# Kernel optimization log

Measured on AMD Instinct MI355X. Metric: run time of the kernel, lower is better.

Reference implementation:

```python
import jax, jax.numpy as jnp
import numpy as np

FEATURE_W = 1.0
TRIPLET_W = 1.0
MARGIN = 0.5
CE_W = 1.0
CE_TEMP = 0.1
DIR_W = 1.0
EPS_VALID = 1e-6
EPS_NORM = 1e-8


def setup_inputs() -> dict:
    key = jax.random.key(0)
    k1, k2, k3, k4, k5 = jax.random.split(key, 5)
    B, C, T, K = 8, 512, 1500, 4096
    return {
        "student_out": jax.random.normal(k1, (B, C, T), dtype=jnp.float32),
        "teacher_out": jax.random.normal(k2, (B, C, T), dtype=jnp.float32),
        "codebook": jax.random.normal(k3, (K, C), dtype=jnp.float32),
        "teacher_codes": jax.random.randint(k4, (B, T), 0, K, dtype=jnp.int64),
        "original_encoder_out": jax.random.normal(k5, (B, C, T), dtype=jnp.float32),
    }


def reference(student_out, teacher_out, codebook, teacher_codes, original_encoder_out):
    B, C, T = student_out.shape
    K = codebook.shape[0]
    N = B * T

    # ---- feature MSE ----
    feature_loss = jnp.mean((student_out - teacher_out) ** 2)

    # ---- triplet with hard negative mining ----
    z = jnp.transpose(student_out, (0, 2, 1)).reshape(N, C)  # (N, C)
    tgt = teacher_codes.reshape(N)
    # squared L2 distances (argmin-equivalent to cdist since sqrt is monotone)
    z2 = jnp.sum(z * z, axis=1, keepdims=True)            # (N, 1)
    c2 = jnp.sum(codebook * codebook, axis=1)             # (K,)
    d2 = z2 - 2.0 * (z @ codebook.T) + c2[None, :]        # (N, K)
    d2 = d2.at[jnp.arange(N), tgt].set(jnp.inf)           # exclude correct code
    hard_idx = jnp.argmin(d2, axis=1)                     # (N,)
    hard_negatives = codebook[hard_idx].reshape(B, T, C)

    anchor = jnp.transpose(teacher_out, (0, 2, 1))        # (B, T, C)
    positive = jnp.transpose(student_out, (0, 2, 1))
    d_pos = jnp.linalg.norm(anchor - positive, axis=-1)   # (B, T)
    d_neg = jnp.linalg.norm(anchor - hard_negatives, axis=-1)
    triplet_loss = jnp.mean(jax.nn.relu(d_pos - d_neg + MARGIN))

    # ---- CE over codebook (negative squared distance logits) ----
    logits = (2.0 * (z @ codebook.T) - c2[None, :]) / CE_TEMP  # (N, K)
    logp = jax.nn.log_softmax(logits, axis=-1)
    ce_loss = -jnp.mean(jnp.take_along_axis(logp, tgt[:, None], axis=1))

    # ---- direction-aware loss ----
    movement = jnp.transpose(student_out - original_encoder_out, (0, 2, 1)).reshape(N, C)
    direction = jnp.transpose(teacher_out - original_encoder_out, (0, 2, 1)).reshape(N, C)
    m_norm = jnp.linalg.norm(movement, axis=-1, keepdims=True)
    d_norm = jnp.linalg.norm(direction, axis=-1, keepdims=True)
    valid = (m_norm[:, 0] > EPS_VALID) & (d_norm[:, 0] > EPS_VALID)  # (N,)
    cos = jnp.sum((movement / (m_norm + EPS_NORM)) * (direction / (d_norm + EPS_NORM)), axis=-1)
    n_valid = jnp.sum(valid)
    dir_cos_loss = jnp.sum(jnp.where(valid, 1.0 - cos, 0.0)) / jnp.maximum(n_valid, 1).astype(cos.dtype)
    dir_mse = jnp.mean((student_out - teacher_out) ** 2)
    direction_loss = dir_mse + 1.0 * dir_cos_loss  # DirectionAwareLoss(direction_weight=1.0)

    total = (FEATURE_W * feature_loss + TRIPLET_W * triplet_loss
             + CE_W * ce_loss + DIR_W * direction_loss)
    return total
```

## Files before the change

kernel.cpp:

```cpp
#include <hip/hip_runtime.h>
#include <math.h>

#define NN 12000
#define NP 12032
#define CCD 512
#define KK 4096
#define TT 1500
#define S20F 28.853900817779268f
#define SC2F 14.426950408889634f
#define LN2F 0.6931471805599453f

typedef float f32x4 __attribute__((ext_vector_type(4)));
typedef __bf16 bf16x8 __attribute__((ext_vector_type(8)));

__device__ __forceinline__ ushort f2bf(float f){
  uint u = __float_as_uint(f);
  uint r = (u + 0x7fffu + ((u >> 16) & 1u)) >> 16;
  return (ushort)r;
}

typedef __attribute__((address_space(1))) const unsigned int g_u32;
typedef __attribute__((address_space(3))) unsigned int l_u32;
__device__ __forceinline__ void gload_lds16(const void* g, void* l){
  __builtin_amdgcn_global_load_lds((g_u32*)g, (l_u32*)l, 16, 0, 0);
}

__global__ __launch_bounds__(256) void k_prep_z(const float* __restrict__ src, ushort* __restrict__ dst){
  __shared__ float tile[64][65];
  int b = blockIdx.z, c0 = blockIdx.y*64, t0 = blockIdx.x*64;
  const float* sb = src + ((size_t)b*CCD + c0)*TT + t0;
  for (int i = 0; i < 16; ++i){
    int e = i*256 + threadIdx.x;
    int cl = e >> 6, tl = e & 63;
    if (t0 + tl < TT) tile[cl][tl] = sb[(size_t)cl*TT + tl];
  }
  __syncthreads();
  for (int i = 0; i < 16; ++i){
    int e = i*256 + threadIdx.x;
    int tl = e >> 6, cl = e & 63;
    if (t0 + tl < TT) dst[((size_t)b*TT + t0 + tl)*CCD + c0 + cl] = f2bf(tile[cl][tl]);
  }
}

__global__ __launch_bounds__(256) void k_prep_cb(const float* __restrict__ cb, ushort* __restrict__ cbsw){
  int id = blockIdx.x*256 + threadIdx.x;
  int l     = id & 63;
  int kstep = (id >> 6) & 15;
  int tile  = id >> 10;
  int code  = tile*16 + (l & 15);
  int cc    = kstep*32 + (l >> 4)*8;
  const float* src = cb + ((size_t)code*CCD + cc);
  float4 v0 = *(const float4*)src;
  float4 v1 = *(const float4*)(src + 4);
  uint4 o;
  o.x = (uint)f2bf(v0.x) | ((uint)f2bf(v0.y) << 16);
  o.y = (uint)f2bf(v0.z) | ((uint)f2bf(v0.w) << 16);
  o.z = (uint)f2bf(v1.x) | ((uint)f2bf(v1.y) << 16);
  o.w = (uint)f2bf(v1.z) | ((uint)f2bf(v1.w) << 16);
  ((uint4*)cbsw)[id] = o;
}

__global__ __launch_bounds__(256) void k_c2(const float* __restrict__ cb, float* __restrict__ c2s){
  int k = blockIdx.x*4 + (threadIdx.x >> 6);
  int lane = threadIdx.x & 63;
  const float4* p = (const float4*)(cb + (size_t)k*CCD);
  float s = 0.f;
  for (int i = lane; i < CCD/4; i += 64){
    float4 v = p[i];
    s += v.x*v.x + v.y*v.y + v.z*v.z + v.w*v.w;
  }
  for (int off=1; off<64; off<<=1) s += __shfl_xor(s, off);
  if (lane == 0) c2s[k] = s * SC2F;
}

__global__ __launch_bounds__(256) void k_dist(const ushort* __restrict__ zbf,
    const ushort* __restrict__ cbsw, const float* __restrict__ c2s,
    const int* __restrict__ codes, float4* __restrict__ pstate){
  __shared__ char cs[2*16384];
  int tid = threadIdx.x, w = tid >> 6, l = tid & 63;
  int lm = l & 15, k16 = l >> 4;
  int yk = blockIdx.x, xb = blockIdx.y;
  int n0 = xb * 128, kb = yk * 512;

  bf16x8 A0[16], A1[16];
  {
    const ushort* a0 = zbf + (size_t)(n0 + w*32 + lm)*CCD + k16*8;
#pragma unroll
    for (int u = 0; u < 16; ++u){
      A0[u] = *(const bf16x8*)(a0 + u*32);
      A1[u] = *(const bf16x8*)(a0 + 16*CCD + u*32);
    }
  }
  int tgt[8];
#pragma unroll
  for (int fi=0; fi<2; ++fi)
#pragma unroll
    for (int r=0; r<4; ++r){
      int n = n0 + w*32 + fi*16 + k16*4 + r;
      tgt[fi*4+r] = (n < NN) ? codes[n] : -1;
    }

  float m2[8], ss[8], bv[8]; int bi[8];
#pragma unroll
  for (int i=0;i<8;++i){ m2[i]=-3.0e38f; ss[i]=0.f; bv[i]=-3.0e38f; bi[i]=0x7fffffff; }

#define STAGE(tile, buf) { \
    const char* tb_ = (const char*)cbsw + ((size_t)(yk*32 + (tile)))*16384; \
    _Pragma("unroll") \
    for (int j_ = 0; j_ < 4; ++j_) \
      gload_lds16(tb_ + j_*4096 + tid*16, (buf) + j_*4096 + tid*16); }

  STAGE(0, cs)
  __syncthreads();

#pragma unroll 2
  for (int t = 0; t < 32; ++t){
    const char* cur = cs + (t & 1)*16384;
    char* nxt = cs + ((t + 1) & 1)*16384;
    if (t < 31) STAGE(t + 1, nxt)

    f32x4 a0e = (f32x4){0.f,0.f,0.f,0.f}, a0o = a0e, a1e = a0e, a1o = a0e;
    const char* pb = cur + l*16;
    __builtin_amdgcn_s_setprio(1);
#pragma unroll
    for (int ks = 0; ks < 16; ks += 2){
      bf16x8 b0 = *(const bf16x8*)(pb + ks*1024);
      bf16x8 b1 = *(const bf16x8*)(pb + ks*1024 + 1024);
      a0e = __builtin_amdgcn_mfma_f32_16x16x32_bf16(A0[ks],   b0, a0e, 0,0,0);
      a1e = __builtin_amdgcn_mfma_f32_16x16x32_bf16(A1[ks],   b0, a1e, 0,0,0);
      a0o = __builtin_amdgcn_mfma_f32_16x16x32_bf16(A0[ks+1], b1, a0o, 0,0,0);
      a1o = __builtin_amdgcn_mfma_f32_16x16x32_bf16(A1[ks+1], b1, a1o, 0,0,0);
    }
    __builtin_amdgcn_s_setprio(0);

    int c0g = kb + t*16 + lm;
    float c2r0 = c2s[c0g];
    f32x4 accf[2];
    accf[0] = a0e + a0o;
    accf[1] = a1e + a1o;
#pragma unroll
    for (int fi=0; fi<2; ++fi)
#pragma unroll
    for (int r=0; r<4; ++r){
      int i8 = fi*4 + r;
      float v0 = fmaf(accf[fi][r], S20F, -c2r0);
      if (c0g != tgt[i8] && v0 > bv[i8]){ bv[i8] = v0; bi[i8] = c0g; }
      float mn = fmaxf(m2[i8], v0);
      ss[i8] = ss[i8]*exp2f(m2[i8]-mn) + exp2f(v0-mn);
      m2[i8] = mn;
    }
    __syncthreads();
  }
#undef STAGE

#pragma unroll
  for (int off = 1; off < 16; off <<= 1){
#pragma unroll
    for (int i=0; i<8; ++i){
      float mo = __shfl_xor(m2[i], off);
      float so = __shfl_xor(ss[i], off);
      float bvo = __shfl_xor(bv[i], off);
      int  bio = __shfl_xor(bi[i], off);
      if (bvo > bv[i] || (bvo == bv[i] && bio < bi[i])){ bv[i] = bvo; bi[i] = bio; }
      float mn = fmaxf(m2[i], mo);
      ss[i] = ss[i]*exp2f(m2[i]-mn) + so*exp2f(mo-mn);
      m2[i] = mn;
    }
  }
  if (lm == 0){
#pragma unroll
    for (int fi=0; fi<2; ++fi)
#pragma unroll
    for (int r=0; r<4; ++r){
      int i8 = fi*4 + r;
      int row = w*32 + fi*16 + k16*4 + r;
      pstate[(size_t)yk*NP + n0 + row] =
          make_float4(m2[i8], ss[i8], bv[i8], __int_as_float(bi[i8]));
    }
  }
}

__global__ __launch_bounds__(256) void k_final(const float* __restrict__ student,
    const float* __restrict__ teacher, const float* __restrict__ orig,
    const float* __restrict__ cb, const float4* __restrict__ pstate,
    const int* __restrict__ codes, const float* __restrict__ c2s,
    float* __restrict__ accs){
  __shared__ float red[6][4][64];
  __shared__ int   sh_hard[64];
  __shared__ float sh_lse[64];
  int tt = threadIdx.x & 63, cg = threadIdx.x >> 6;
  int n = blockIdx.x*64 + tt;
  bool ok = (n < NN);
  if (cg == 0){
    float m=-3.0e38f, s=0.f, bvv=-3.0e38f; int bii=0x7fffffff;
    if (ok){
      for (int sp = 0; sp < 8; ++sp){
        float4 p = pstate[(size_t)sp*NP + n];
        int pb = __float_as_int(p.w);
        if (p.z > bvv || (p.z == bvv && pb < bii)){ bvv = p.z; bii = pb; }
        float mn = fmaxf(m, p.x);
        s = s*exp2f(m - mn) + p.y*exp2f(p.x - mn);
        m = mn;
      }
    } else { bii = 0; s = 1.f; m = 0.f; }
    sh_hard[tt] = bii;
    sh_lse[tt]  = m + log2f(s);
  }
  __syncthreads();
  float dp2=0,dn2=0,mm=0,dd=0,md=0,dt=0;
  int tg = 0;
  if (ok){
    int hn = sh_hard[tt]; tg = codes[n];
    int b = n / TT, t = n - b*TT;
    size_t base = (size_t)b*CCD*TT + t;
    const float* ch = cb + (size_t)hn*CCD;
    const float* ct = cb + (size_t)tg*CCD;
    for (int c = cg*128; c < cg*128+128; ++c){
      float sv = student[base + (size_t)c*TT];
      float tv = teacher[base + (size_t)c*TT];
      float ov = orig[base + (size_t)c*TT];
      float cv = ch[c], wv = ct[c];
      float u = sv - tv; dp2 = fmaf(u,u,dp2);
      float v = tv - cv; dn2 = fmaf(v,v,dn2);
      float mv = sv - ov, dv = tv - ov;
      mm = fmaf(mv,mv,mm); dd = fmaf(dv,dv,dd); md = fmaf(mv,dv,md);
      dt = fmaf(sv, wv, dt);
    }
  }
  red[0][cg][tt]=dp2; red[1][cg][tt]=dn2; red[2][cg][tt]=mm;
  red[3][cg][tt]=dd;  red[4][cg][tt]=md;  red[5][cg][tt]=dt;
  __syncthreads();
  if (cg == 0){
    dp2 = red[0][0][tt]+red[0][1][tt]+red[0][2][tt]+red[0][3][tt];
    dn2 = red[1][0][tt]+red[1][1][tt]+red[1][2][tt]+red[1][3][tt];
    mm  = red[2][0][tt]+red[2][1][tt]+red[2][2][tt]+red[2][3][tt];
    dd  = red[3][0][tt]+red[3][1][tt]+red[3][2][tt]+red[3][3][tt];
    md  = red[4][0][tt]+red[4][1][tt]+red[4][2][tt]+red[4][3][tt];
    dt  = red[5][0][tt]+red[5][1][tt]+red[5][2][tt]+red[5][3][tt];
    float trip=0.f, dc=0.f, nv=0.f, ce=0.f;
    if (ok){
      float dpos = sqrtf(dp2), dneg = sqrtf(dn2);
      trip = fmaxf(dpos - dneg + 0.5f, 0.f);
      float mn = sqrtf(mm), dnn = sqrtf(dd);
      bool valid = (mn > 1e-6f) && (dnn > 1e-6f);
      float cosv = md / ((mn + 1e-8f)*(dnn + 1e-8f));
      if (valid){ dc = 1.f - cosv; nv = 1.f; }
      ce = sh_lse[tt] - (fmaf(dt, S20F, -c2s[tg]));
    }
    for (int off=1; off<64; off<<=1){
      trip += __shfl_xor(trip,off);
      dc   += __shfl_xor(dc,off);
      nv   += __shfl_xor(nv,off);
      dp2  += __shfl_xor(dp2,off);
      ce   += __shfl_xor(ce,off);
    }
    if (tt == 0){
      atomicAdd(&accs[0], trip); atomicAdd(&accs[1], dc);
      atomicAdd(&accs[2], nv);   atomicAdd(&accs[3], dp2);
      atomicAdd(&accs[4], ce);
    }
  }
}

__global__ void k_total(const float* __restrict__ accs, float* __restrict__ out){
  float feat = accs[3] / 6144000.f;
  float trip = accs[0] / (float)NN;
  float ce   = (accs[4] / (float)NN) * LN2F;
  float nv   = accs[2] < 1.f ? 1.f : accs[2];
  float dc   = accs[1] / nv;
  out[0] = 2.f*feat + trip + ce + dc;
}

extern "C" void kernel_launch(void* const* d_in, const int* in_sizes, int n_in,
                              void* d_out, int out_size, void* d_ws, size_t ws_size,
                              hipStream_t stream){
  const float* student = (const float*)d_in[0];
  const float* teacher = (const float*)d_in[1];
  const float* cb      = (const float*)d_in[2];
  const int*   codes   = (const int*)d_in[3];
  const float* orig    = (const float*)d_in[4];

  char* ws = (char*)d_ws;
  ushort* zbf    = (ushort*)(ws);
  ushort* cbsw   = (ushort*)(ws + 12320768);
  float*  c2s    = (float*)(ws + 16515072);
  float4* pstate = (float4*)(ws + 16531456);
  float*  accs   = (float*)(ws + 18071552);
  hipMemsetAsync(ws + 18071552, 0, 64, stream);
  k_prep_cb<<<1024, 256, 0, stream>>>(cb, cbsw);
  k_c2<<<1024, 256, 0, stream>>>(cb, c2s);
  k_prep_z<<<dim3(24, 8, 8), 256, 0, stream>>>(student, zbf);
  k_dist<<<dim3(8, 94), 256, 0, stream>>>(zbf, cbsw, c2s, codes, pstate);
  k_final<<<188, 256, 0, stream>>>(student, teacher, orig, cb, pstate, codes, c2s, accs);
  k_total<<<1, 1, 0, stream>>>(accs, (float*)d_out);
}
```

Before: 164.3 us.

## Software-pipeline distance epilogue with MFMA, capture target logit, fuse c2 into prep

```diff
diff --git a/kernel.cpp b/kernel.cpp
--- a/kernel.cpp
+++ b/kernel.cpp
@@ -13,6 +13,15 @@
 typedef float f32x4 __attribute__((ext_vector_type(4)));
 typedef __bf16 bf16x8 __attribute__((ext_vector_type(8)));
 
+#if __has_builtin(__builtin_amdgcn_exp2f)
+#define EXP2(x) __builtin_amdgcn_exp2f(x)
+#else
+static __device__ __forceinline__ float exp2_asm(float x){
+  float r; asm("v_exp_f32 %0, %1" : "=v"(r) : "v"(x)); return r;
+}
+#define EXP2(x) exp2_asm(x)
+#endif
+
 __device__ __forceinline__ ushort f2bf(float f){
   uint u = __float_as_uint(f);
   uint r = (u + 0x7fffu + ((u >> 16) & 1u)) >> 16;
@@ -42,7 +51,8 @@
   }
 }
 
-__global__ __launch_bounds__(256) void k_prep_cb(const float* __restrict__ cb, ushort* __restrict__ cbsw){
+__global__ __launch_bounds__(256) void k_prep_cb(const float* __restrict__ cb,
+    ushort* __restrict__ cbsw, float* __restrict__ c2s){
   int id = blockIdx.x*256 + threadIdx.x;
   int l     = id & 63;
   int kstep = (id >> 6) & 15;
@@ -58,24 +68,17 @@
   o.z = (uint)f2bf(v1.x) | ((uint)f2bf(v1.y) << 16);
   o.w = (uint)f2bf(v1.z) | ((uint)f2bf(v1.w) << 16);
   ((uint4*)cbsw)[id] = o;
-}
-
-__global__ __launch_bounds__(256) void k_c2(const float* __restrict__ cb, float* __restrict__ c2s){
-  int k = blockIdx.x*4 + (threadIdx.x >> 6);
-  int lane = threadIdx.x & 63;
-  const float4* p = (const float4*)(cb + (size_t)k*CCD);
-  float s = 0.f;
-  for (int i = lane; i < CCD/4; i += 64){
-    float4 v = p[i];
-    s += v.x*v.x + v.y*v.y + v.z*v.z + v.w*v.w;
-  }
-  for (int off=1; off<64; off<<=1) s += __shfl_xor(s, off);
-  if (lane == 0) c2s[k] = s * SC2F;
+  float s = v0.x*v0.x + v0.y*v0.y + v0.z*v0.z + v0.w*v0.w
+          + v1.x*v1.x + v1.y*v1.y + v1.z*v1.z + v1.w*v1.w;
+  s += __shfl_xor(s, 16);
+  s += __shfl_xor(s, 32);
+  if ((l >> 4) == 0) atomicAdd(&c2s[code], s * SC2F);
 }
 
 __global__ __launch_bounds__(256) void k_dist(const ushort* __restrict__ zbf,
     const ushort* __restrict__ cbsw, const float* __restrict__ c2s,
-    const int* __restrict__ codes, float4* __restrict__ pstate){
+    const int* __restrict__ codes, float4* __restrict__ pstate,
+    float* __restrict__ pltgt){
   __shared__ char cs[2*16384];
   int tid = threadIdx.x, w = tid >> 6, l = tid & 63;
   int lm = l & 15, k16 = l >> 4;
@@ -100,9 +103,9 @@
       tgt[fi*4+r] = (n < NN) ? codes[n] : -1;
     }
 
-  float m2[8], ss[8], bv[8]; int bi[8];
-#pragma unroll
-  for (int i=0;i<8;++i){ m2[i]=-3.0e38f; ss[i]=0.f; bv[i]=-3.0e38f; bi[i]=0x7fffffff; }
+  float m2[8], ss[8], bv[8], lt[8]; int bi[8];
+#pragma unroll
+  for (int i=0;i<8;++i){ m2[i]=-3.0e38f; ss[i]=0.f; bv[i]=-3.0e38f; lt[i]=-3.0e38f; bi[i]=0x7fffffff; }
 
 #define STAGE(tile, buf) { \
     const char* tb_ = (const char*)cbsw + ((size_t)(yk*32 + (tile)))*16384; \
@@ -110,10 +113,21 @@
     for (int j_ = 0; j_ < 4; ++j_) \
       gload_lds16(tb_ + j_*4096 + tid*16, (buf) + j_*4096 + tid*16); }
 
+#define EPI(p) { \
+    float v0_ = fmaf(((p) < 4 ? pA0[(p) & 3] : pA1[(p) & 3]), S20F, -pc2); \
+    if (pcol != tgt[(p)] && v0_ > bv[(p)]){ bv[(p)] = v0_; bi[(p)] = pcol; } \
+    if (pcol == tgt[(p)]) lt[(p)] = v0_; \
+    float mn_ = fmaxf(m2[(p)], v0_); \
+    ss[(p)] = ss[(p)]*EXP2(m2[(p)]-mn_) + EXP2(v0_-mn_); \
+    m2[(p)] = mn_; }
+
   STAGE(0, cs)
   __syncthreads();
 
-#pragma unroll 2
+  f32x4 pA0 = (f32x4){0.f,0.f,0.f,0.f}, pA1 = (f32x4){0.f,0.f,0.f,0.f};
+  int pcol = 0; float pc2 = 0.f;
+
+#pragma unroll
   for (int t = 0; t < 32; ++t){
     const char* cur = cs + (t & 1)*16384;
     char* nxt = cs + ((t + 1) & 1)*16384;
@@ -123,34 +137,25 @@
     const char* pb = cur + l*16;
     __builtin_amdgcn_s_setprio(1);
 #pragma unroll
-    for (int ks = 0; ks < 16; ks += 2){
-      bf16x8 b0 = *(const bf16x8*)(pb + ks*1024);
-      bf16x8 b1 = *(const bf16x8*)(pb + ks*1024 + 1024);
-      a0e = __builtin_amdgcn_mfma_f32_16x16x32_bf16(A0[ks],   b0, a0e, 0,0,0);
-      a1e = __builtin_amdgcn_mfma_f32_16x16x32_bf16(A1[ks],   b0, a1e, 0,0,0);
-      a0o = __builtin_amdgcn_mfma_f32_16x16x32_bf16(A0[ks+1], b1, a0o, 0,0,0);
-      a1o = __builtin_amdgcn_mfma_f32_16x16x32_bf16(A1[ks+1], b1, a1o, 0,0,0);
+    for (int p = 0; p < 8; ++p){
+      bf16x8 b0 = *(const bf16x8*)(pb + p*2048);
+      bf16x8 b1 = *(const bf16x8*)(pb + p*2048 + 1024);
+      a0e = __builtin_amdgcn_mfma_f32_16x16x32_bf16(A0[2*p],   b0, a0e, 0,0,0);
+      a1e = __builtin_amdgcn_mfma_f32_16x16x32_bf16(A1[2*p],   b0, a1e, 0,0,0);
+      a0o = __builtin_amdgcn_mfma_f32_16x16x32_bf16(A0[2*p+1], b1, a0o, 0,0,0);
+      a1o = __builtin_amdgcn_mfma_f32_16x16x32_bf16(A1[2*p+1], b1, a1o, 0,0,0);
+      if (t > 0) EPI(p)
     }
     __builtin_amdgcn_s_setprio(0);
 
-    int c0g = kb + t*16 + lm;
-    float c2r0 = c2s[c0g];
-    f32x4 accf[2];
-    accf[0] = a0e + a0o;
-    accf[1] = a1e + a1o;
-#pragma unroll
-    for (int fi=0; fi<2; ++fi)
-#pragma unroll
-    for (int r=0; r<4; ++r){
-      int i8 = fi*4 + r;
-      float v0 = fmaf(accf[fi][r], S20F, -c2r0);
-      if (c0g != tgt[i8] && v0 > bv[i8]){ bv[i8] = v0; bi[i8] = c0g; }
-      float mn = fmaxf(m2[i8], v0);
-      ss[i8] = ss[i8]*exp2f(m2[i8]-mn) + exp2f(v0-mn);
-      m2[i8] = mn;
-    }
+    pA0 = a0e + a0o; pA1 = a1e + a1o;
+    pcol = kb + t*16 + lm;
+    pc2  = c2s[pcol];
     __syncthreads();
   }
+#pragma unroll
+  for (int p = 0; p < 8; ++p) EPI(p)
+#undef EPI
 #undef STAGE
 
 #pragma unroll
@@ -161,9 +166,11 @@
       float so = __shfl_xor(ss[i], off);
       float bvo = __shfl_xor(bv[i], off);
       int  bio = __shfl_xor(bi[i], off);
+      float lto = __shfl_xor(lt[i], off);
       if (bvo > bv[i] || (bvo == bv[i] && bio < bi[i])){ bv[i] = bvo; bi[i] = bio; }
+      lt[i] = fmaxf(lt[i], lto);
       float mn = fmaxf(m2[i], mo);
-      ss[i] = ss[i]*exp2f(m2[i]-mn) + so*exp2f(mo-mn);
+      ss[i] = ss[i]*EXP2(m2[i]-mn) + so*EXP2(mo-mn);
       m2[i] = mn;
     }
   }
@@ -176,6 +183,7 @@
       int row = w*32 + fi*16 + k16*4 + r;
       pstate[(size_t)yk*NP + n0 + row] =
           make_float4(m2[i8], ss[i8], bv[i8], __int_as_float(bi[i8]));
+      pltgt[(size_t)yk*NP + n0 + row] = lt[i8];
     }
   }
 }
@@ -183,52 +191,49 @@
 __global__ __launch_bounds__(256) void k_final(const float* __restrict__ student,
     const float* __restrict__ teacher, const float* __restrict__ orig,
     const float* __restrict__ cb, const float4* __restrict__ pstate,
-    const int* __restrict__ codes, const float* __restrict__ c2s,
-    float* __restrict__ accs){
-  __shared__ float red[6][4][64];
+    const float* __restrict__ pltgt, float* __restrict__ accs){
+  __shared__ float red[5][4][64];
   __shared__ int   sh_hard[64];
-  __shared__ float sh_lse[64];
+  __shared__ float sh_ce[64];
   int tt = threadIdx.x & 63, cg = threadIdx.x >> 6;
   int n = blockIdx.x*64 + tt;
   bool ok = (n < NN);
   if (cg == 0){
-    float m=-3.0e38f, s=0.f, bvv=-3.0e38f; int bii=0x7fffffff;
+    float m=-3.0e38f, s=0.f, bvv=-3.0e38f, ltv=-3.0e38f; int bii=0x7fffffff;
     if (ok){
       for (int sp = 0; sp < 8; ++sp){
         float4 p = pstate[(size_t)sp*NP + n];
         int pb = __float_as_int(p.w);
         if (p.z > bvv || (p.z == bvv && pb < bii)){ bvv = p.z; bii = pb; }
+        ltv = fmaxf(ltv, pltgt[(size_t)sp*NP + n]);
         float mn = fmaxf(m, p.x);
-        s = s*exp2f(m - mn) + p.y*exp2f(p.x - mn);
+        s = s*EXP2(m - mn) + p.y*EXP2(p.x - mn);
         m = mn;
       }
-    } else { bii = 0; s = 1.f; m = 0.f; }
+    } else { bii = 0; s = 1.f; m = 0.f; ltv = 0.f; }
     sh_hard[tt] = bii;
-    sh_lse[tt]  = m + log2f(s);
+    sh_ce[tt]   = (m + log2f(s)) - ltv;
   }
   __syncthreads();
-  float dp2=0,dn2=0,mm=0,dd=0,md=0,dt=0;
-  int tg = 0;
+  float dp2=0,dn2=0,mm=0,dd=0,md=0;
   if (ok){
-    int hn = sh_hard[tt]; tg = codes[n];
+    int hn = sh_hard[tt];
     int b = n / TT, t = n - b*TT;
     size_t base = (size_t)b*CCD*TT + t;
     const float* ch = cb + (size_t)hn*CCD;
-    const float* ct = cb + (size_t)tg*CCD;
     for (int c = cg*128; c < cg*128+128; ++c){
       float sv = student[base + (size_t)c*TT];
       float tv = teacher[base + (size_t)c*TT];
       float ov = orig[base + (size_t)c*TT];
-      float cv = ch[c], wv = ct[c];
+      float cv = ch[c];
       float u = sv - tv; dp2 = fmaf(u,u,dp2);
       float v = tv - cv; dn2 = fmaf(v,v,dn2);
       float mv = sv - ov, dv = tv - ov;
       mm = fmaf(mv,mv,mm); dd = fmaf(dv,dv,dd); md = fmaf(mv,dv,md);
-      dt = fmaf(sv, wv, dt);
     }
   }
   red[0][cg][tt]=dp2; red[1][cg][tt]=dn2; red[2][cg][tt]=mm;
-  red[3][cg][tt]=dd;  red[4][cg][tt]=md;  red[5][cg][tt]=dt;
+  red[3][cg][tt]=dd;  red[4][cg][tt]=md;
   __syncthreads();
   if (cg == 0){
     dp2 = red[0][0][tt]+red[0][1][tt]+red[0][2][tt]+red[0][3][tt];
@@ -236,7 +241,6 @@
     mm  = red[2][0][tt]+red[2][1][tt]+red[2][2][tt]+red[2][3][tt];
     dd  = red[3][0][tt]+red[3][1][tt]+red[3][2][tt]+red[3][3][tt];
     md  = red[4][0][tt]+red[4][1][tt]+red[4][2][tt]+red[4][3][tt];
-    dt  = red[5][0][tt]+red[5][1][tt]+red[5][2][tt]+red[5][3][tt];
     float trip=0.f, dc=0.f, nv=0.f, ce=0.f;
     if (ok){
       float dpos = sqrtf(dp2), dneg = sqrtf(dn2);
@@ -245,7 +249,7 @@
       bool valid = (mn > 1e-6f) && (dnn > 1e-6f);
       float cosv = md / ((mn + 1e-8f)*(dnn + 1e-8f));
       if (valid){ dc = 1.f - cosv; nv = 1.f; }
-      ce = sh_lse[tt] - (fmaf(dt, S20F, -c2s[tg]));
+      ce = sh_ce[tt];
     }
     for (int off=1; off<64; off<<=1){
       trip += __shfl_xor(trip,off);
@@ -285,12 +289,13 @@
   ushort* cbsw   = (ushort*)(ws + 12320768);
   float*  c2s    = (float*)(ws + 16515072);
   float4* pstate = (float4*)(ws + 16531456);
-  float*  accs   = (float*)(ws + 18071552);
-  hipMemsetAsync(ws + 18071552, 0, 64, stream);
-  k_prep_cb<<<1024, 256, 0, stream>>>(cb, cbsw);
-  k_c2<<<1024, 256, 0, stream>>>(cb, c2s);
+  float*  pltgt  = (float*)(ws + 18071552);
+  float*  accs   = (float*)(ws + 18456576);
+  hipMemsetAsync(ws + 18456576, 0, 64, stream);
+  hipMemsetAsync(c2s, 0, 16384, stream);
+  k_prep_cb<<<1024, 256, 0, stream>>>(cb, cbsw, c2s);
   k_prep_z<<<dim3(24, 8, 8), 256, 0, stream>>>(student, zbf);
-  k_dist<<<dim3(8, 94), 256, 0, stream>>>(zbf, cbsw, c2s, codes, pstate);
-  k_final<<<188, 256, 0, stream>>>(student, teacher, orig, cb, pstate, codes, c2s, accs);
+  k_dist<<<dim3(8, 94), 256, 0, stream>>>(zbf, cbsw, c2s, codes, pstate, pltgt);
+  k_final<<<188, 256, 0, stream>>>(student, teacher, orig, cb, pstate, pltgt, accs);
   k_total<<<1, 1, 0, stream>>>(accs, (float*)d_out);
 }
```

New measurement: 181.6 us. 1.11x slower.
